# Kernel optimization log

Hardware: AMD Instinct MI355X
Metric: run time of the kernel (lower is better)

The kernel has to match this reference:

```python
import jax, jax.numpy as jnp
import numpy as np

B, S, D, H = 4, 2048, 1024, 16
DK = D // H  # 64


def setup_inputs() -> dict:
    key = jax.random.key(0)
    ks = jax.random.split(key, 11)
    scale = 1.0 / np.sqrt(D)
    inp = {
        "query": jax.random.normal(ks[0], (B, S, D), jnp.float32),
        "key": jax.random.normal(ks[1], (B, S, D), jnp.float32),
        "value": jax.random.normal(ks[2], (B, S, D), jnp.float32),
        "Wq": jax.random.normal(ks[3], (D, D), jnp.float32) * scale,
        "bq": jnp.zeros((D,), jnp.float32),
        "Wk": jax.random.normal(ks[4], (D, D), jnp.float32) * scale,
        "bk": jnp.zeros((D,), jnp.float32),
        "Wv": jax.random.normal(ks[5], (D, D), jnp.float32) * scale,
        "bv": jnp.zeros((D,), jnp.float32),
        "Wo": jax.random.normal(ks[6], (D, D), jnp.float32) * scale,
        "bo": jnp.zeros((D,), jnp.float32),
    }
    return inp


def reference(query, key, value, Wq, bq, Wk, bk, Wv, bv, Wo, bo):
    # Projections: torch Linear computes x @ W.T + b; here W is stored as (in, out)
    def split_heads(x):
        return x.reshape(B, S, H, DK).transpose(0, 2, 1, 3)  # [B,H,S,DK]

    Q = split_heads(query @ Wq + bq)
    K = split_heads(key @ Wk + bk)
    V = split_heads(value @ Wv + bv)

    scores = jnp.einsum("bhqd,bhkd->bhqk", Q, K) / jnp.sqrt(jnp.float32(DK))
    attn = jax.nn.softmax(scores, axis=-1)  # [B,H,S,S]
    ctx = jnp.einsum("bhqk,bhkd->bhqd", attn, V)
    ctx = ctx.transpose(0, 2, 1, 3).reshape(B, S, D)
    return ctx @ Wo + bo
```

## Files before the change

### kernel.cpp

```cpp
#include <hip/hip_runtime.h>
#include <hip/hip_bf16.h>
#include <cstdint>

#define DEV __device__ __forceinline__

typedef __bf16 bf16x8 __attribute__((ext_vector_type(8)));
typedef float f32x4 __attribute__((ext_vector_type(4)));
typedef unsigned short u16;
typedef unsigned short u16x8 __attribute__((ext_vector_type(8)));
typedef unsigned short u16x4 __attribute__((ext_vector_type(4)));

#if defined(__has_builtin) && __has_builtin(__builtin_amdgcn_exp2f)
#define EXP2F(x) __builtin_amdgcn_exp2f(x)
#else
#define EXP2F(x) exp2f(x)
#endif

static constexpr float QSCALE = 0.125f * 1.44269504088896340736f;

DEV u16 f2bf(float f) {
  uint32_t x = __builtin_bit_cast(uint32_t, f);
  x += 0x7fffu + ((x >> 16) & 1u);
  return (u16)(x >> 16);
}

DEV u16x4 pack4(float a, float b, float c, float d) {
  union { __hip_bfloat162 h[2]; u16x4 u; } r;
  r.h[0] = __float22bfloat162_rn(make_float2(a, b));
  r.h[1] = __float22bfloat162_rn(make_float2(c, d));
  return r.u;
}

DEV u16x8 cvt8(const float* p) {
  const float4 v0 = *(const float4*)p;
  const float4 v1 = *(const float4*)(p + 4);
  union { __hip_bfloat162 h[4]; u16x8 u; } r;
  r.h[0] = __float22bfloat162_rn(make_float2(v0.x, v0.y));
  r.h[1] = __float22bfloat162_rn(make_float2(v0.z, v0.w));
  r.h[2] = __float22bfloat162_rn(make_float2(v1.x, v1.y));
  r.h[3] = __float22bfloat162_rn(make_float2(v1.z, v1.w));
  return r.u;
}

DEV f32x4 mfma16(bf16x8 a, bf16x8 b, f32x4 c) {
  return __builtin_amdgcn_mfma_f32_16x16x32_bf16(a, b, c, 0, 0, 0);
}

DEV void gll16(const void* g, const void* l) {
  __builtin_amdgcn_global_load_lds(
      (const __attribute__((address_space(1))) uint32_t*)g,
      (__attribute__((address_space(3))) uint32_t*)l, 16, 0, 0);
}

__global__ __launch_bounds__(256) void cvt_kernel(
    const float* __restrict__ X0, const float* __restrict__ X1,
    const float* __restrict__ X2, u16* __restrict__ Y0,
    u16* __restrict__ Y1, u16* __restrict__ Y2) {
  const float* X = (blockIdx.z == 0) ? X0 : (blockIdx.z == 1) ? X1 : X2;
  u16* Y = (blockIdx.z == 0) ? Y0 : (blockIdx.z == 1) ? Y1 : Y2;
  const size_t i = ((size_t)blockIdx.x * 256 + threadIdx.x) * 8;
  *(u16x8*)(Y + i) = cvt8(X + i);
}

__global__ __launch_bounds__(256) void wtrans_kernel(
    const float* __restrict__ W0, const float* __restrict__ W1,
    const float* __restrict__ W2, const float* __restrict__ W3,
    u16* __restrict__ T0, u16* __restrict__ T1,
    u16* __restrict__ T2, u16* __restrict__ T3) {
  const float* W = (blockIdx.z == 0) ? W0 : (blockIdx.z == 1) ? W1 : (blockIdx.z == 2) ? W2 : W3;
  u16* T = (blockIdx.z == 0) ? T0 : (blockIdx.z == 1) ? T1 : (blockIdx.z == 2) ? T2 : T3;
  __shared__ float tile[32][33];
  const int tid = threadIdx.x;
  const int r = tid >> 3, c0 = (tid & 7) * 4;
  const float4 v = *(const float4*)(W + (size_t)(blockIdx.y * 32 + r) * 1024 + blockIdx.x * 32 + c0);
  tile[r][c0 + 0] = v.x; tile[r][c0 + 1] = v.y; tile[r][c0 + 2] = v.z; tile[r][c0 + 3] = v.w;
  __syncthreads();
  u16x4 o = pack4(tile[c0 + 0][r], tile[c0 + 1][r], tile[c0 + 2][r], tile[c0 + 3][r]);
  *(u16x4*)(T + (size_t)(blockIdx.x * 32 + r) * 1024 + blockIdx.y * 32 + c0) = o;
}

__global__ __launch_bounds__(512) void gemm_qkv_kernel(
    const u16* __restrict__ X0, const u16* __restrict__ X1,
    const u16* __restrict__ X2, const u16* __restrict__ W0t,
    const u16* __restrict__ W1t, const u16* __restrict__ W2t,
    const float* __restrict__ b0, const float* __restrict__ b1,
    const float* __restrict__ b2, u16* __restrict__ O0,
    u16* __restrict__ O1, u16* __restrict__ O2) {
  __shared__ u16 As[2][128 * 32];
  __shared__ u16 Bs[2][128 * 32];
  const int z = blockIdx.z;
  const u16* X = (z == 0) ? X0 : (z == 1) ? X1 : X2;
  const u16* Wt = (z == 0) ? W0t : (z == 1) ? W1t : W2t;
  const float* bias = (z == 0) ? b0 : (z == 1) ? b1 : b2;
  u16* O = (z == 0) ? O0 : (z == 1) ? O1 : O2;
  const float scale = (z == 0) ? QSCALE : 1.0f;

  const int nb = blockIdx.y * 8 + blockIdx.x;
  const int sb = (nb & 7) * 64 + (nb >> 3);
  const int bxs = sb & 7, bys = sb >> 3;

  const int tid = threadIdx.x;
  const int w = tid >> 6, lane = tid & 63, ln = lane & 15, quad = lane >> 4;
  const int wm = w >> 1, wn = w & 1;
  const int bm = bys * 128, bn = bxs * 128;

  f32x4 acc[2][4];
#pragma unroll
  for (int i = 0; i < 2; i++)
#pragma unroll
    for (int j = 0; j < 4; j++) acc[i][j] = f32x4{0.f, 0.f, 0.f, 0.f};

  const int lrow = w * 16 + (lane >> 2);
  const u16* ga = X + (size_t)(bm + lrow) * 1024 + (lane & 3) * 8;
  const u16* gb = Wt + (size_t)(bn + lrow) * 1024 + (lane & 3) * 8;
  const u16* lA = (const u16*)&As[0][0] + w * 512;
  const u16* lB = (const u16*)&Bs[0][0] + w * 512;

  gll16(ga, lA);
  gll16(gb, lB);

#pragma unroll 2
  for (int kt = 0; kt < 32; ++kt) {
    __syncthreads();
    const int cur = (kt & 1) << 12;
    if (kt < 31) {
      const int nxt = 4096 - cur;
      gll16(ga + (size_t)(kt + 1) * 32, lA + nxt);
      gll16(gb + (size_t)(kt + 1) * 32, lB + nxt);
    }

    bf16x8 af[2], bf[4];
#pragma unroll
    for (int i = 0; i < 2; i++)
      af[i] = *(const bf16x8*)&As[0][cur + (wm * 32 + i * 16 + ln) * 32 + quad * 8];
#pragma unroll
    for (int j = 0; j < 4; j++)
      bf[j] = *(const bf16x8*)&Bs[0][cur + (wn * 64 + j * 16 + ln) * 32 + quad * 8];
#pragma unroll
    for (int i = 0; i < 2; i++)
#pragma unroll
      for (int j = 0; j < 4; j++) acc[i][j] = mfma16(af[i], bf[j], acc[i][j]);
  }

#pragma unroll
  for (int j = 0; j < 4; j++) {
    const int n = bn + wn * 64 + j * 16 + ln;
    const float bv = bias[n];
#pragma unroll
    for (int i = 0; i < 2; i++) {
      const int m0 = bm + wm * 32 + i * 16 + quad * 4;
      const int h = n >> 6, dk = n & 63;
      if (z != 2) {
#pragma unroll
        for (int r = 0; r < 4; r++) {
          const int m = m0 + r, b = m >> 11, s = m & 2047;
          O[((size_t)(b * 16 + h) * 2048 + s) * 64 + dk] = f2bf((acc[i][j][r] + bv) * scale);
        }
      } else {
        const int b = m0 >> 11, s0 = m0 & 2047;
        u16x4 pk = pack4(acc[i][j][0] + bv, acc[i][j][1] + bv,
                         acc[i][j][2] + bv, acc[i][j][3] + bv);
        *(u16x4*)(O + (size_t)((b * 16 + h) * 64 + dk) * 2048 + s0) = pk;
      }
    }
  }
}

__global__ __launch_bounds__(512) void gemm_o_kernel(
    const u16* __restrict__ X, const u16* __restrict__ Wt,
    const float* __restrict__ bias, float* __restrict__ Out) {
  __shared__ u16 As[2][128 * 32];
  __shared__ u16 Bs[2][128 * 32];
  const int nb = blockIdx.y * 8 + blockIdx.x;
  const int sb = (nb & 7) * 64 + (nb >> 3);
  const int bxs = sb & 7, bys = sb >> 3;

  const int tid = threadIdx.x;
  const int w = tid >> 6, lane = tid & 63, ln = lane & 15, quad = lane >> 4;
  const int wm = w >> 1, wn = w & 1;
  const int bm = bys * 128, bn = bxs * 128;

  f32x4 acc[2][4];
#pragma unroll
  for (int i = 0; i < 2; i++)
#pragma unroll
    for (int j = 0; j < 4; j++) acc[i][j] = f32x4{0.f, 0.f, 0.f, 0.f};

  const int lrow = w * 16 + (lane >> 2);
  const u16* ga = X + (size_t)(bm + lrow) * 1024 + (lane & 3) * 8;
  const u16* gb = Wt + (size_t)(bn + lrow) * 1024 + (lane & 3) * 8;
  const u16* lA = (const u16*)&As[0][0] + w * 512;
  const u16* lB = (const u16*)&Bs[0][0] + w * 512;

  gll16(ga, lA);
  gll16(gb, lB);

#pragma unroll 2
  for (int kt = 0; kt < 32; ++kt) {
    __syncthreads();
    const int cur = (kt & 1) << 12;
    if (kt < 31) {
      const int nxt = 4096 - cur;
      gll16(ga + (size_t)(kt + 1) * 32, lA + nxt);
      gll16(gb + (size_t)(kt + 1) * 32, lB + nxt);
    }

    bf16x8 af[2], bf[4];
#pragma unroll
    for (int i = 0; i < 2; i++)
      af[i] = *(const bf16x8*)&As[0][cur + (wm * 32 + i * 16 + ln) * 32 + quad * 8];
#pragma unroll
    for (int j = 0; j < 4; j++)
      bf[j] = *(const bf16x8*)&Bs[0][cur + (wn * 64 + j * 16 + ln) * 32 + quad * 8];
#pragma unroll
    for (int i = 0; i < 2; i++)
#pragma unroll
      for (int j = 0; j < 4; j++) acc[i][j] = mfma16(af[i], bf[j], acc[i][j]);
  }

#pragma unroll
  for (int j = 0; j < 4; j++) {
    const int n = bn + wn * 64 + j * 16 + ln;
    const float bv = bias[n];
#pragma unroll
    for (int i = 0; i < 2; i++) {
      const int m0 = bm + wm * 32 + i * 16 + quad * 4;
#pragma unroll
      for (int r = 0; r < 4; r++) Out[(size_t)(m0 + r) * 1024 + n] = acc[i][j][r] + bv;
    }
  }
}

__global__ __launch_bounds__(512) void fattn_kernel(
    const u16* __restrict__ Q, const u16* __restrict__ K,
    const u16* __restrict__ V, u16* __restrict__ ctx) {
  __shared__ u16 Ks[2][64 * 64];
  __shared__ u16 Vs[2][64 * 64];
  __shared__ u16 Ps[8 * 16 * 64];

  const int tid = threadIdx.x;
  const int w = tid >> 6, lane = tid & 63, ln = lane & 15, quad = lane >> 4;

  const int nb = blockIdx.y * 16 + blockIdx.x;
  const int sb = (nb & 7) * 128 + (nb >> 3);
  const int qt = sb & 15, bh = sb >> 4;
  const size_t base = (size_t)bh * 2048 * 64;

  const int sr = tid >> 3, sc = (tid & 7) * 8;
  const int swc = ((tid & 7) ^ (sr & 7)) * 8;
  const int sw = ln & 7;

  bf16x8 qf[2];
#pragma unroll
  for (int ks = 0; ks < 2; ks++)
    qf[ks] = *(const bf16x8*)(Q + base + (size_t)(qt * 128 + w * 16 + ln) * 64 + ks * 32 + quad * 8);

  f32x4 lv = f32x4{0.f, 0.f, 0.f, 0.f};
  f32x4 accO[4];
#pragma unroll
  for (int d = 0; d < 4; d++) accO[d] = f32x4{0.f, 0.f, 0.f, 0.f};

  {
    u16x8 kr = *(const u16x8*)(K + base + (size_t)sr * 64 + sc);
    u16x8 vr = *(const u16x8*)(V + base + (size_t)sr * 2048 + sc);
    *(u16x8*)&Ks[0][sr * 64 + swc] = kr;
    *(u16x8*)&Vs[0][sr * 64 + swc] = vr;
  }

  for (int t = 0; t < 32; ++t) {
    __syncthreads();
    const int cur = (t & 1) << 12;

    u16x8 krn, vrn;
    if (t < 31) {
      krn = *(const u16x8*)(K + base + (size_t)((t + 1) * 64 + sr) * 64 + sc);
      vrn = *(const u16x8*)(V + base + (size_t)sr * 2048 + (t + 1) * 64 + sc);
    }

    f32x4 s[4];
#pragma unroll
    for (int i = 0; i < 4; i++) s[i] = f32x4{0.f, 0.f, 0.f, 0.f};
    __builtin_amdgcn_s_setprio(1);
#pragma unroll
    for (int i = 0; i < 4; i++) {
#pragma unroll
      for (int ks = 0; ks < 2; ks++) {
        const bf16x8 kf = *(const bf16x8*)&Ks[0][cur + (i * 16 + ln) * 64 + ((4 * ks + quad) ^ sw) * 8];
        s[i] = mfma16(kf, qf[ks], s[i]);
      }
    }
    __builtin_amdgcn_s_setprio(0);

#pragma unroll
    for (int i = 0; i < 4; i++) {
#pragma unroll
      for (int r = 0; r < 4; r++) s[i][r] = EXP2F(s[i][r]);
      lv += s[i];
      *(u16x4*)&Ps[(w * 16 + ln) * 64 +
                   (((2 * i + (quad >> 1)) ^ sw) * 8) + (quad & 1) * 4] =
          pack4(s[i][0], s[i][1], s[i][2], s[i][3]);
    }

    __builtin_amdgcn_s_setprio(1);
#pragma unroll
    for (int ks = 0; ks < 2; ks++) {
      const bf16x8 pf = *(const bf16x8*)&Ps[(w * 16 + ln) * 64 + ((4 * ks + quad) ^ sw) * 8];
#pragma unroll
      for (int dkt = 0; dkt < 4; dkt++) {
        const bf16x8 vf = *(const bf16x8*)&Vs[0][cur + (dkt * 16 + ln) * 64 + ((4 * ks + quad) ^ sw) * 8];
        accO[dkt] = mfma16(vf, pf, accO[dkt]);
      }
    }
    __builtin_amdgcn_s_setprio(0);

    if (t < 31) {
      const int nxt = 4096 - cur;
      *(u16x8*)&Ks[0][nxt + sr * 64 + swc] = krn;
      *(u16x8*)&Vs[0][nxt + sr * 64 + swc] = vrn;
    }
  }

  const int b = bh >> 4, h = bh & 15;
  float l = (lv[0] + lv[1]) + (lv[2] + lv[3]);
  l += __shfl_xor(l, 16, 64);
  l += __shfl_xor(l, 32, 64);
  const float linv = 1.0f / l;
  const int qs = qt * 128 + w * 16 + ln;
#pragma unroll
  for (int dkt = 0; dkt < 4; dkt++) {
    u16x4 pk = pack4(accO[dkt][0] * linv, accO[dkt][1] * linv,
                     accO[dkt][2] * linv, accO[dkt][3] * linv);
    *(u16x4*)(ctx + (size_t)(b * 2048 + qs) * 1024 + h * 64 + dkt * 16 + quad * 4) = pk;
  }
}

extern "C" void kernel_launch(void* const* d_in, const int* in_sizes, int n_in,
                              void* d_out, int out_size, void* d_ws, size_t ws_size,
                              hipStream_t stream) {
  const float* q  = (const float*)d_in[0];
  const float* k  = (const float*)d_in[1];
  const float* v  = (const float*)d_in[2];
  const float* Wq = (const float*)d_in[3];
  const float* bq = (const float*)d_in[4];
  const float* Wk = (const float*)d_in[5];
  const float* bk = (const float*)d_in[6];
  const float* Wv = (const float*)d_in[7];
  const float* bv = (const float*)d_in[8];
  const float* Wo = (const float*)d_in[9];
  const float* bo = (const float*)d_in[10];

  u16* Wtq = (u16*)d_ws;
  u16* Wtk = Wtq + 1024 * 1024;
  u16* Wtv = Wtk + 1024 * 1024;
  u16* Wto = Wtv + 1024 * 1024;
  u16* qb  = Wto + 1024 * 1024;
  u16* kb  = qb + 8192 * 1024;
  u16* vb  = kb + 8192 * 1024;
  u16* Qb  = vb + 8192 * 1024;
  u16* Kb  = Qb + 8192 * 1024;
  u16* Vtb = Kb + 8192 * 1024;
  u16* Cb  = qb;

  cvt_kernel<<<dim3(4096, 1, 3), 256, 0, stream>>>(q, k, v, qb, kb, vb);
  wtrans_kernel<<<dim3(32, 32, 4), 256, 0, stream>>>(Wq, Wk, Wv, Wo, Wtq, Wtk, Wtv, Wto);

  gemm_qkv_kernel<<<dim3(8, 64, 3), 512, 0, stream>>>(
      qb, kb, vb, Wtq, Wtk, Wtv, bq, bk, bv, Qb, Kb, Vtb);

  fattn_kernel<<<dim3(16, 64), 512, 0, stream>>>(Qb, Kb, Vtb, Cb);

  gemm_o_kernel<<<dim3(8, 64), 512, 0, stream>>>(Cb, Wto, bo, (float*)d_out);
}
```

Measured before the change: 343.6 us.

## Keep attention probabilities in registers via permlane swaps; transpose V-projection MFMA

The attention kernel no longer writes exp'd scores to shared memory and reads them back as MFMA operands. It packs them into bf16 pairs and rearranges them across lanes with v_permlane32/16_swap, which removes the P LDS buffer and its round trip. The kernel also gets an occupancy hint in launch_bounds. For the V projection the MFMA operands are swapped so each lane holds consecutive output columns, and the transposed store layout changes accordingly. The risks are getting the permlane mapping wrong and losing coalescing in the V-projection writes, which are now scalar 2-byte stores strided in n.

Result: no change. 348.4 us (+1.4%).

```diff
diff --git a/kernel.cpp b/kernel.cpp
--- a/kernel.cpp
+++ b/kernel.cpp
@@ -28,6 +28,12 @@
   union { __hip_bfloat162 h[2]; u16x4 u; } r;
   r.h[0] = __float22bfloat162_rn(make_float2(a, b));
   r.h[1] = __float22bfloat162_rn(make_float2(c, d));
+  return r.u;
+}
+
+DEV uint32_t pkbf(float a, float b) {
+  union { __hip_bfloat162 h; uint32_t u; } r;
+  r.h = __float22bfloat162_rn(make_float2(a, b));
   return r.u;
 }
 
@@ -136,31 +142,50 @@
 #pragma unroll
     for (int j = 0; j < 4; j++)
       bf[j] = *(const bf16x8*)&Bs[0][cur + (wn * 64 + j * 16 + ln) * 32 + quad * 8];
-#pragma unroll
-    for (int i = 0; i < 2; i++)
-#pragma unroll
-      for (int j = 0; j < 4; j++) acc[i][j] = mfma16(af[i], bf[j], acc[i][j]);
-  }
-
-#pragma unroll
-  for (int j = 0; j < 4; j++) {
-    const int n = bn + wn * 64 + j * 16 + ln;
-    const float bv = bias[n];
-#pragma unroll
-    for (int i = 0; i < 2; i++) {
-      const int m0 = bm + wm * 32 + i * 16 + quad * 4;
+    if (z != 2) {
+#pragma unroll
+      for (int i = 0; i < 2; i++)
+#pragma unroll
+        for (int j = 0; j < 4; j++) acc[i][j] = mfma16(af[i], bf[j], acc[i][j]);
+    } else {
+#pragma unroll
+      for (int i = 0; i < 2; i++)
+#pragma unroll
+        for (int j = 0; j < 4; j++) acc[i][j] = mfma16(bf[j], af[i], acc[i][j]);
+    }
+  }
+
+  if (z != 2) {
+#pragma unroll
+    for (int j = 0; j < 4; j++) {
+      const int n = bn + wn * 64 + j * 16 + ln;
+      const float bv = bias[n];
       const int h = n >> 6, dk = n & 63;
-      if (z != 2) {
+#pragma unroll
+      for (int i = 0; i < 2; i++) {
+        const int m0 = bm + wm * 32 + i * 16 + quad * 4;
 #pragma unroll
         for (int r = 0; r < 4; r++) {
           const int m = m0 + r, b = m >> 11, s = m & 2047;
           O[((size_t)(b * 16 + h) * 2048 + s) * 64 + dk] = f2bf((acc[i][j][r] + bv) * scale);
         }
-      } else {
-        const int b = m0 >> 11, s0 = m0 & 2047;
-        u16x4 pk = pack4(acc[i][j][0] + bv, acc[i][j][1] + bv,
-                         acc[i][j][2] + bv, acc[i][j][3] + bv);
-        *(u16x4*)(O + (size_t)((b * 16 + h) * 64 + dk) * 2048 + s0) = pk;
+      }
+    }
+  } else {
+#pragma unroll
+    for (int j = 0; j < 4; j++) {
+      const int n0 = bn + wn * 64 + j * 16 + quad * 4;
+      const f32x4 bv4 = *(const f32x4*)&bias[n0];
+#pragma unroll
+      for (int i = 0; i < 2; i++) {
+        const int m = bm + wm * 32 + i * 16 + ln;
+        const int b = m >> 11, s = m & 2047;
+#pragma unroll
+        for (int r = 0; r < 4; r++) {
+          const int n = n0 + r;
+          O[((size_t)(b * 16 + (n >> 6)) * 64 + (n & 63)) * 2048 + s] =
+              f2bf(acc[i][j][r] + bv4[r]);
+        }
       }
     }
   }
@@ -231,12 +256,11 @@
   }
 }
 
-__global__ __launch_bounds__(512) void fattn_kernel(
+__global__ __launch_bounds__(512, 8) void fattn_kernel(
     const u16* __restrict__ Q, const u16* __restrict__ K,
     const u16* __restrict__ V, u16* __restrict__ ctx) {
   __shared__ u16 Ks[2][64 * 64];
   __shared__ u16 Vs[2][64 * 64];
-  __shared__ u16 Ps[8 * 16 * 64];
 
   const int tid = threadIdx.x;
   const int w = tid >> 6, lane = tid & 63, ln = lane & 15, quad = lane >> 4;
@@ -291,24 +315,37 @@
     }
     __builtin_amdgcn_s_setprio(0);
 
+    uint32_t pw[4][2];
 #pragma unroll
     for (int i = 0; i < 4; i++) {
 #pragma unroll
       for (int r = 0; r < 4; r++) s[i][r] = EXP2F(s[i][r]);
       lv += s[i];
-      *(u16x4*)&Ps[(w * 16 + ln) * 64 +
-                   (((2 * i + (quad >> 1)) ^ sw) * 8) + (quad & 1) * 4] =
-          pack4(s[i][0], s[i][1], s[i][2], s[i][3]);
+      pw[i][0] = pkbf(s[i][0], s[i][1]);
+      pw[i][1] = pkbf(s[i][2], s[i][3]);
+    }
+
+    bf16x8 pf[2];
+#pragma unroll
+    for (int ks = 0; ks < 2; ks++) {
+      uint32_t a0 = pw[2 * ks][0], b0 = pw[2 * ks + 1][0];
+      uint32_t a1 = pw[2 * ks][1], b1 = pw[2 * ks + 1][1];
+      asm("v_permlane32_swap_b32 %0, %1" : "+v"(a0), "+v"(b0));
+      asm("v_permlane16_swap_b32 %0, %1" : "+v"(a0), "+v"(b0));
+      asm("v_permlane32_swap_b32 %0, %1" : "+v"(a1), "+v"(b1));
+      asm("v_permlane16_swap_b32 %0, %1" : "+v"(a1), "+v"(b1));
+      union { uint32_t u[4]; bf16x8 v; } pu;
+      pu.u[0] = a0; pu.u[1] = a1; pu.u[2] = b0; pu.u[3] = b1;
+      pf[ks] = pu.v;
     }
 
     __builtin_amdgcn_s_setprio(1);
 #pragma unroll
     for (int ks = 0; ks < 2; ks++) {
-      const bf16x8 pf = *(const bf16x8*)&Ps[(w * 16 + ln) * 64 + ((4 * ks + quad) ^ sw) * 8];
 #pragma unroll
       for (int dkt = 0; dkt < 4; dkt++) {
         const bf16x8 vf = *(const bf16x8*)&Vs[0][cur + (dkt * 16 + ln) * 64 + ((4 * ks + quad) ^ sw) * 8];
-        accO[dkt] = mfma16(vf, pf, accO[dkt]);
+        accO[dkt] = mfma16(vf, pf[ks], accO[dkt]);
       }
     }
     __builtin_amdgcn_s_setprio(0);
```

## Fuse fp32-to-bf16 input conversion into QKV GEMM A-tile loads

Applied to the files above, without the earlier changes.

Removes the separate conversion kernel and has the QKV GEMM load fp32 activations directly, converting them to bf16 in registers and storing them to shared memory with register-prefetch double buffering. It also swaps the MFMA operand order for the V projection so that the transposed V output is written with lanes along the sequence dimension. The aim is to avoid writing and re-reading the bf16 copies of the three activation tensors. In exchange the A path loses the async global-to-LDS loads, raises register pressure, and drops the loop unroll.

After: 387.8 us. +12.9%, slower.

```diff
diff --git a/kernel.cpp b/kernel.cpp
--- a/kernel.cpp
+++ b/kernel.cpp
@@ -31,9 +31,7 @@
   return r.u;
 }
 
-DEV u16x8 cvt8(const float* p) {
-  const float4 v0 = *(const float4*)p;
-  const float4 v1 = *(const float4*)(p + 4);
+DEV u16x8 cvt8v(float4 v0, float4 v1) {
   union { __hip_bfloat162 h[4]; u16x8 u; } r;
   r.h[0] = __float22bfloat162_rn(make_float2(v0.x, v0.y));
   r.h[1] = __float22bfloat162_rn(make_float2(v0.z, v0.w));
@@ -50,16 +48,6 @@
   __builtin_amdgcn_global_load_lds(
       (const __attribute__((address_space(1))) uint32_t*)g,
       (__attribute__((address_space(3))) uint32_t*)l, 16, 0, 0);
-}
-
-__global__ __launch_bounds__(256) void cvt_kernel(
-    const float* __restrict__ X0, const float* __restrict__ X1,
-    const float* __restrict__ X2, u16* __restrict__ Y0,
-    u16* __restrict__ Y1, u16* __restrict__ Y2) {
-  const float* X = (blockIdx.z == 0) ? X0 : (blockIdx.z == 1) ? X1 : X2;
-  u16* Y = (blockIdx.z == 0) ? Y0 : (blockIdx.z == 1) ? Y1 : Y2;
-  const size_t i = ((size_t)blockIdx.x * 256 + threadIdx.x) * 8;
-  *(u16x8*)(Y + i) = cvt8(X + i);
 }
 
 __global__ __launch_bounds__(256) void wtrans_kernel(
@@ -80,8 +68,8 @@
 }
 
 __global__ __launch_bounds__(512) void gemm_qkv_kernel(
-    const u16* __restrict__ X0, const u16* __restrict__ X1,
-    const u16* __restrict__ X2, const u16* __restrict__ W0t,
+    const float* __restrict__ X0, const float* __restrict__ X1,
+    const float* __restrict__ X2, const u16* __restrict__ W0t,
     const u16* __restrict__ W1t, const u16* __restrict__ W2t,
     const float* __restrict__ b0, const float* __restrict__ b1,
     const float* __restrict__ b2, u16* __restrict__ O0,
@@ -89,7 +77,7 @@
   __shared__ u16 As[2][128 * 32];
   __shared__ u16 Bs[2][128 * 32];
   const int z = blockIdx.z;
-  const u16* X = (z == 0) ? X0 : (z == 1) ? X1 : X2;
+  const float* X = (z == 0) ? X0 : (z == 1) ? X1 : X2;
   const u16* Wt = (z == 0) ? W0t : (z == 1) ? W1t : W2t;
   const float* bias = (z == 0) ? b0 : (z == 1) ? b1 : b2;
   u16* O = (z == 0) ? O0 : (z == 1) ? O1 : O2;
@@ -110,22 +98,28 @@
 #pragma unroll
     for (int j = 0; j < 4; j++) acc[i][j] = f32x4{0.f, 0.f, 0.f, 0.f};
 
+  const int ar = tid >> 2, ac = (tid & 3) * 8;
+  const float* gaf = X + (size_t)(bm + ar) * 1024 + ac;
   const int lrow = w * 16 + (lane >> 2);
-  const u16* ga = X + (size_t)(bm + lrow) * 1024 + (lane & 3) * 8;
   const u16* gb = Wt + (size_t)(bn + lrow) * 1024 + (lane & 3) * 8;
-  const u16* lA = (const u16*)&As[0][0] + w * 512;
   const u16* lB = (const u16*)&Bs[0][0] + w * 512;
 
-  gll16(ga, lA);
+  {
+    const float4 a0 = *(const float4*)gaf;
+    const float4 a1 = *(const float4*)(gaf + 4);
+    *(u16x8*)&As[0][ar * 32 + ac] = cvt8v(a0, a1);
+  }
   gll16(gb, lB);
 
-#pragma unroll 2
   for (int kt = 0; kt < 32; ++kt) {
     __syncthreads();
     const int cur = (kt & 1) << 12;
+    const int nxt = 4096 - cur;
+
+    float4 a0n, a1n;
     if (kt < 31) {
-      const int nxt = 4096 - cur;
-      gll16(ga + (size_t)(kt + 1) * 32, lA + nxt);
+      a0n = *(const float4*)(gaf + (size_t)(kt + 1) * 32);
+      a1n = *(const float4*)(gaf + (size_t)(kt + 1) * 32 + 4);
       gll16(gb + (size_t)(kt + 1) * 32, lB + nxt);
     }
 
@@ -136,31 +130,54 @@
 #pragma unroll
     for (int j = 0; j < 4; j++)
       bf[j] = *(const bf16x8*)&Bs[0][cur + (wn * 64 + j * 16 + ln) * 32 + quad * 8];
-#pragma unroll
-    for (int i = 0; i < 2; i++)
-#pragma unroll
-      for (int j = 0; j < 4; j++) acc[i][j] = mfma16(af[i], bf[j], acc[i][j]);
-  }
-
-#pragma unroll
-  for (int j = 0; j < 4; j++) {
-    const int n = bn + wn * 64 + j * 16 + ln;
-    const float bv = bias[n];
-#pragma unroll
-    for (int i = 0; i < 2; i++) {
-      const int m0 = bm + wm * 32 + i * 16 + quad * 4;
+    if (z != 2) {
+#pragma unroll
+      for (int i = 0; i < 2; i++)
+#pragma unroll
+        for (int j = 0; j < 4; j++) acc[i][j] = mfma16(af[i], bf[j], acc[i][j]);
+    } else {
+#pragma unroll
+      for (int i = 0; i < 2; i++)
+#pragma unroll
+        for (int j = 0; j < 4; j++) acc[i][j] = mfma16(bf[j], af[i], acc[i][j]);
+    }
+
+    if (kt < 31) {
+      *(u16x8*)&As[0][nxt + ar * 32 + ac] = cvt8v(a0n, a1n);
+    }
+  }
+
+  if (z != 2) {
+#pragma unroll
+    for (int j = 0; j < 4; j++) {
+      const int n = bn + wn * 64 + j * 16 + ln;
+      const float bv = bias[n];
       const int h = n >> 6, dk = n & 63;
-      if (z != 2) {
+#pragma unroll
+      for (int i = 0; i < 2; i++) {
+        const int m0 = bm + wm * 32 + i * 16 + quad * 4;
 #pragma unroll
         for (int r = 0; r < 4; r++) {
           const int m = m0 + r, b = m >> 11, s = m & 2047;
           O[((size_t)(b * 16 + h) * 2048 + s) * 64 + dk] = f2bf((acc[i][j][r] + bv) * scale);
         }
-      } else {
-        const int b = m0 >> 11, s0 = m0 & 2047;
-        u16x4 pk = pack4(acc[i][j][0] + bv, acc[i][j][1] + bv,
-                         acc[i][j][2] + bv, acc[i][j][3] + bv);
-        *(u16x4*)(O + (size_t)((b * 16 + h) * 64 + dk) * 2048 + s0) = pk;
+      }
+    }
+  } else {
+#pragma unroll
+    for (int j = 0; j < 4; j++) {
+      const int n0 = bn + wn * 64 + j * 16 + quad * 4;
+      const f32x4 bv4 = *(const f32x4*)&bias[n0];
+#pragma unroll
+      for (int i = 0; i < 2; i++) {
+        const int m = bm + wm * 32 + i * 16 + ln;
+        const int b = m >> 11, s = m & 2047;
+#pragma unroll
+        for (int r = 0; r < 4; r++) {
+          const int n = n0 + r;
+          O[((size_t)(b * 16 + (n >> 6)) * 64 + (n & 63)) * 2048 + s] =
+              f2bf(acc[i][j][r] + bv4[r]);
+        }
       }
     }
   }
@@ -353,19 +370,15 @@
   u16* Wtk = Wtq + 1024 * 1024;
   u16* Wtv = Wtk + 1024 * 1024;
   u16* Wto = Wtv + 1024 * 1024;
-  u16* qb  = Wto + 1024 * 1024;
-  u16* kb  = qb + 8192 * 1024;
-  u16* vb  = kb + 8192 * 1024;
-  u16* Qb  = vb + 8192 * 1024;
+  u16* Qb  = Wto + 1024 * 1024;
   u16* Kb  = Qb + 8192 * 1024;
   u16* Vtb = Kb + 8192 * 1024;
-  u16* Cb  = qb;
-
-  cvt_kernel<<<dim3(4096, 1, 3), 256, 0, stream>>>(q, k, v, qb, kb, vb);
+  u16* Cb  = Vtb + 8192 * 1024;
+
   wtrans_kernel<<<dim3(32, 32, 4), 256, 0, stream>>>(Wq, Wk, Wv, Wo, Wtq, Wtk, Wtv, Wto);
 
   gemm_qkv_kernel<<<dim3(8, 64, 3), 512, 0, stream>>>(
-      qb, kb, vb, Wtq, Wtk, Wtv, bq, bk, bv, Qb, Kb, Vtb);
+      q, k, v, Wtq, Wtk, Wtv, bq, bk, bv, Qb, Kb, Vtb);
 
   fattn_kernel<<<dim3(16, 64), 512, 0, stream>>>(Qb, Kb, Vtb, Cb);
 
```
